# Kernel optimization log

Hardware: AMD Instinct MI355X
Metric: run time of the kernel (lower is better)

Reference implementation:

```python
import jax, jax.numpy as jnp
import numpy as np

B, N1, N2, C1, C2, MLP_OUT = 16, 4096, 1024, 128, 256, 256


def setup_inputs() -> dict:
    key = jax.random.key(0)
    k = jax.random.split(key, 8)
    xyz1 = jax.random.normal(k[0], (B, N1, 3), dtype=jnp.float32)
    feat1 = jax.random.normal(k[1], (B, N1, C1), dtype=jnp.float32)
    xyz2 = jax.random.normal(k[2], (B, N2, 3), dtype=jnp.float32)
    feat2 = jax.random.normal(k[3], (B, N2, C2), dtype=jnp.float32)
    d_in = C1 + C2
    W1 = jax.random.normal(k[4], (d_in, MLP_OUT), dtype=jnp.float32) / np.sqrt(d_in)
    b1 = jnp.zeros((MLP_OUT,), dtype=jnp.float32)
    W2 = jax.random.normal(k[5], (MLP_OUT, MLP_OUT), dtype=jnp.float32) / np.sqrt(MLP_OUT)
    b2 = jnp.zeros((MLP_OUT,), dtype=jnp.float32)
    return {"xyz1": xyz1, "feat1": feat1, "xyz2": xyz2, "feat2": feat2,
            "W1": W1, "b1": b1, "W2": W2, "b2": b2}


def reference(xyz1, feat1, xyz2, feat2, W1, b1, W2, b2):
    # squared pairwise distances [B, N1, N2]
    dists = jnp.sum((xyz1[:, :, None, :] - xyz2[:, None, :, :]) ** 2, axis=-1)
    # 3 nearest neighbors (smallest distances)
    neg_d3, idx = jax.lax.top_k(-dists, 3)      # [B, N1, 3]
    d3 = jnp.maximum(-neg_d3, 1e-10)
    w = 1.0 / d3
    w = w / jnp.sum(w, axis=-1, keepdims=True)   # [B, N1, 3]
    # gather neighbor features: [B, N1, 3, C2]
    neighbor_feats = jax.vmap(lambda f, i: f[i])(feat2, idx)
    interpolated = jnp.sum(w[..., None] * neighbor_feats, axis=2)  # [B, N1, C2]
    new_feat = jnp.concatenate([interpolated, feat1], axis=-1)     # [B, N1, C2+C1]
    h = jax.nn.relu(new_feat @ W1 + b1)
    return jax.nn.relu(h @ W2 + b2)
```

## Files before the change

kernel.cpp:

```cpp
#include <hip/hip_runtime.h>
#include <cstdint>
#include <cstddef>

typedef unsigned short ushort_t;
typedef unsigned int uint_t;

typedef __bf16 bf16x8 __attribute__((ext_vector_type(8)));
typedef float floatx4 __attribute__((ext_vector_type(4)));

#define B_ 16
#define N1_ 4096
#define N2_ 1024
#define C1_ 128
#define C2_ 256
#define DIN_ 384
#define DOUT_ 256
#define M_ (B_ * N1_)


__device__ __forceinline__ ushort_t f2bf(float f) {
  unsigned int u = __builtin_bit_cast(unsigned int, f);
  u = (u + 0x7fffu + ((u >> 16) & 1u)) >> 16;
  return (ushort_t)u;
}


__global__ __launch_bounds__(256) void prep_kernel(
    const float* __restrict__ W1, const float* __restrict__ W2,
    ushort_t* __restrict__ W1s, ushort_t* __restrict__ W2s) {
  int e = blockIdx.x * 256 + threadIdx.x;
  if (e < DOUT_ * DIN_) {
    int kk = e & 31, n = (e >> 5) & 255, t = e >> 13;
    W1s[e] = f2bf(W1[(size_t)(t * 32 + kk) * DOUT_ + n]);
  }
  if (e < DOUT_ * DOUT_) {
    int kk = e & 31, n = (e >> 5) & 255, t = e >> 13;
    W2s[e] = f2bf(W2[(size_t)(t * 32 + kk) * DOUT_ + n]);
  }
}


__device__ __forceinline__ void ins_exact(float& s0, float& s1, float& s2,
                                          int& i0, int& i1, int& i2,
                                          float d, int p) {
  float ns2 = __builtin_amdgcn_fmed3f(d, s1, s2);
  float ns1 = __builtin_amdgcn_fmed3f(d, s0, s1);
  float ns0 = fminf(d, s0);
  bool c0 = d < s0, c1 = d < s1, c2 = d < s2;
  i2 = c1 ? i1 : (c2 ? p : i2);
  i1 = c0 ? i0 : (c1 ? p : i1);
  i0 = c0 ? p : i0;
  s0 = ns0; s1 = ns1; s2 = ns2;
}

__device__ __forceinline__ void ins_merge(float& s0, float& s1, float& s2,
                                          int& i0, int& i1, int& i2,
                                          float e, int j) {
  bool t0 = (e < s0) || (e == s0 && j < i0);
  bool t1 = (e < s1) || (e == s1 && j < i1);
  bool t2 = (e < s2) || (e == s2 && j < i2);
  s2 = t1 ? s1 : (t2 ? e : s2);
  i2 = t1 ? i1 : (t2 ? j : i2);
  s1 = t0 ? s0 : (t1 ? e : s1);
  i1 = t0 ? i0 : (t1 ? j : i1);
  s0 = t0 ? e : s0;
  i0 = t0 ? j : i0;
}

__global__ __launch_bounds__(256) void knn_kernel(
    const float* __restrict__ xyz1, const float* __restrict__ xyz2,
    int* __restrict__ idx_out, float* __restrict__ w_out) {
  __shared__ float4 xs4[N2_];
  int b = blockIdx.x >> 6;
  int n1base = (blockIdx.x & 63) << 6;
  const float* p2 = xyz2 + (size_t)b * N2_ * 3;
  for (int i = threadIdx.x; i < N2_; i += 256) {
    const float* s = p2 + 3 * i;
    xs4[i] = make_float4(s[0], s[1], s[2], 0.0f);
  }
  __syncthreads();

  int g = threadIdx.x >> 3;
  int sub = threadIdx.x & 7;
  int rowA = b * N1_ + n1base + g;
  int rowB = rowA + 32;
  const float* pa = xyz1 + (size_t)rowA * 3;
  const float* pb = xyz1 + (size_t)rowB * 3;
  float ax = pa[0], ay = pa[1], az = pa[2];
  float bx = pb[0], by = pb[1], bz = pb[2];

  float as0 = 3.0e38f, as1 = 3.0e38f, as2 = 3.0e38f;
  float bs0 = 3.0e38f, bs1 = 3.0e38f, bs2 = 3.0e38f;
  int ai0 = 0, ai1 = 0, ai2 = 0;
  int bi0 = 0, bi1 = 0, bi2 = 0;

  int p = sub;
#pragma unroll 8
  for (int t = 0; t < N2_ / 8; ++t) {
    float4 qv = xs4[p];
    {
      float dx = ax - qv.x, dy = ay - qv.y, dz = az - qv.z;
      float d = dx * dx + dy * dy + dz * dz;
      ins_exact(as0, as1, as2, ai0, ai1, ai2, d, p);
    }
    {
      float dx = bx - qv.x, dy = by - qv.y, dz = bz - qv.z;
      float d = dx * dx + dy * dy + dz * dz;
      ins_exact(bs0, bs1, bs2, bi0, bi1, bi2, d, p);
    }
    p += 8;
  }

#pragma unroll
  for (int mm = 1; mm <= 4; mm <<= 1) {
    {
      float e0 = __shfl_xor(as0, mm), e1 = __shfl_xor(as1, mm), e2 = __shfl_xor(as2, mm);
      int j0 = __shfl_xor(ai0, mm), j1 = __shfl_xor(ai1, mm), j2 = __shfl_xor(ai2, mm);
      ins_merge(as0, as1, as2, ai0, ai1, ai2, e0, j0);
      ins_merge(as0, as1, as2, ai0, ai1, ai2, e1, j1);
      ins_merge(as0, as1, as2, ai0, ai1, ai2, e2, j2);
    }
    {
      float e0 = __shfl_xor(bs0, mm), e1 = __shfl_xor(bs1, mm), e2 = __shfl_xor(bs2, mm);
      int j0 = __shfl_xor(bi0, mm), j1 = __shfl_xor(bi1, mm), j2 = __shfl_xor(bi2, mm);
      ins_merge(bs0, bs1, bs2, bi0, bi1, bi2, e0, j0);
      ins_merge(bs0, bs1, bs2, bi0, bi1, bi2, e1, j1);
      ins_merge(bs0, bs1, bs2, bi0, bi1, bi2, e2, j2);
    }
  }

  if (sub == 0) {
    {
      float r0 = 1.0f / fmaxf(as0, 1e-10f);
      float r1 = 1.0f / fmaxf(as1, 1e-10f);
      float r2 = 1.0f / fmaxf(as2, 1e-10f);
      float s = 1.0f / (r0 + r1 + r2);
      int base = rowA * 3;
      idx_out[base + 0] = ai0;
      idx_out[base + 1] = ai1;
      idx_out[base + 2] = ai2;
      w_out[base + 0] = r0 * s;
      w_out[base + 1] = r1 * s;
      w_out[base + 2] = r2 * s;
    }
    {
      float r0 = 1.0f / fmaxf(bs0, 1e-10f);
      float r1 = 1.0f / fmaxf(bs1, 1e-10f);
      float r2 = 1.0f / fmaxf(bs2, 1e-10f);
      float s = 1.0f / (r0 + r1 + r2);
      int base = rowB * 3;
      idx_out[base + 0] = bi0;
      idx_out[base + 1] = bi1;
      idx_out[base + 2] = bi2;
      w_out[base + 0] = r0 * s;
      w_out[base + 1] = r1 * s;
      w_out[base + 2] = r2 * s;
    }
  }
}


__global__ __launch_bounds__(256, 2) void fused_kernel(
    const float* __restrict__ feat1, const float* __restrict__ feat2,
    const int* __restrict__ idx, const float* __restrict__ w,
    const ushort_t* __restrict__ W1s, const float* __restrict__ b1,
    const ushort_t* __restrict__ W2s, const float* __restrict__ b2,
    float* __restrict__ out) {
  __shared__ ushort_t As[64 * 384];
  const int tid = threadIdx.x;
  const int wave = tid >> 6;
  const int lane = tid & 63;
  const int m = lane & 15;
  const int q = lane >> 4;
  const int row0 = blockIdx.x * 64;
  const int b = row0 >> 12;

#pragma unroll 4
  for (int it = 0; it < 16; ++it) {
    int rl = wave * 16 + it;
    int row = row0 + rl;
    const int* ip = idx + (size_t)row * 3;
    const float* wp = w + (size_t)row * 3;
    int i0 = ip[0], i1 = ip[1], i2 = ip[2];
    float w0 = wp[0], w1 = wp[1], w2 = wp[2];

    const float4* f0 = (const float4*)(feat2 + ((size_t)b * N2_ + i0) * C2_);
    const float4* f1 = (const float4*)(feat2 + ((size_t)b * N2_ + i1) * C2_);
    const float4* f2 = (const float4*)(feat2 + ((size_t)b * N2_ + i2) * C2_);
    float4 a = f0[lane];
    float4 c = f1[lane];
    float4 d = f2[lane];
    float vx = w0 * a.x + w1 * c.x + w2 * d.x;
    float vy = w0 * a.y + w1 * c.y + w2 * d.y;
    float vz = w0 * a.z + w1 * c.z + w2 * d.z;
    float vw = w0 * a.w + w1 * c.w + w2 * d.w;
    uint_t lo = (uint_t)f2bf(vx) | ((uint_t)f2bf(vy) << 16);
    uint_t hi = (uint_t)f2bf(vz) | ((uint_t)f2bf(vw) << 16);
    int e = (lane >> 3) * 2048 + rl * 32 + ((4 * lane) & 31);
    *(uint2*)&As[e] = make_uint2(lo, hi);

    float2 t1 = ((const float2*)(feat1 + (size_t)row * C1_))[lane];
    uint_t pk = (uint_t)f2bf(t1.x) | ((uint_t)f2bf(t1.y) << 16);
    int e1 = (8 + (lane >> 4)) * 2048 + rl * 32 + ((2 * lane) & 31);
    *(uint_t*)&As[e1] = pk;
  }
  __syncthreads();

  const int b_off = (wave * 64 + m) * 32 + q * 8;
  const int a_base = m * 32 + q * 8;

  floatx4 acc[4][4];
#pragma unroll
  for (int i = 0; i < 4; ++i)
#pragma unroll
    for (int j = 0; j < 4; ++j) acc[i][j] = (floatx4)0.0f;

  {
    bf16x8 bf0[4], bf1[4], af[4];
#pragma unroll
    for (int j = 0; j < 4; ++j)
      bf0[j] = *(const bf16x8*)(W1s + b_off + j * 512);
#pragma unroll
    for (int t = 0; t < 12; t += 2) {
#pragma unroll
      for (int j = 0; j < 4; ++j)
        bf1[j] = *(const bf16x8*)(W1s + (size_t)(t + 1) * 8192 + b_off + j * 512);
#pragma unroll
      for (int i = 0; i < 4; ++i)
        af[i] = *(const bf16x8*)&As[t * 2048 + a_base + i * 512];
#pragma unroll
      for (int i = 0; i < 4; ++i)
#pragma unroll
        for (int j = 0; j < 4; ++j)
          acc[i][j] = __builtin_amdgcn_mfma_f32_16x16x32_bf16(af[i], bf0[j],
                                                              acc[i][j], 0, 0, 0);
      if (t + 2 < 12) {
#pragma unroll
        for (int j = 0; j < 4; ++j)
          bf0[j] = *(const bf16x8*)(W1s + (size_t)(t + 2) * 8192 + b_off + j * 512);
      }
#pragma unroll
      for (int i = 0; i < 4; ++i)
        af[i] = *(const bf16x8*)&As[(t + 1) * 2048 + a_base + i * 512];
#pragma unroll
      for (int i = 0; i < 4; ++i)
#pragma unroll
        for (int j = 0; j < 4; ++j)
          acc[i][j] = __builtin_amdgcn_mfma_f32_16x16x32_bf16(af[i], bf1[j],
                                                              acc[i][j], 0, 0, 0);
    }
  }
  __syncthreads();

  ushort_t* HS = As;
#pragma unroll
  for (int j = 0; j < 4; ++j) {
    int col = wave * 64 + j * 16 + m;
    float bv = b1[col];
    int cb = (col >> 3) & 3;
    int tb = (col >> 5) * 2048 + (col & 7);
#pragma unroll
    for (int i = 0; i < 4; ++i)
#pragma unroll
      for (int r = 0; r < 4; ++r) {
        int row = i * 16 + q * 4 + r;
        float v = acc[i][j][r] + bv;
        v = v > 0.0f ? v : 0.0f;
        int ch = cb ^ ((row >> 2) & 3);
        HS[tb + row * 32 + ch * 8] = f2bf(v);
      }
  }
  __syncthreads();

  floatx4 acc2[4][4];
#pragma unroll
  for (int i = 0; i < 4; ++i)
#pragma unroll
    for (int j = 0; j < 4; ++j) acc2[i][j] = (floatx4)0.0f;

  {
    bf16x8 bf0[4], bf1[4], af[4];
#pragma unroll
    for (int j = 0; j < 4; ++j)
      bf0[j] = *(const bf16x8*)(W2s + b_off + j * 512);
#pragma unroll
    for (int t = 0; t < 8; t += 2) {
#pragma unroll
      for (int j = 0; j < 4; ++j)
        bf1[j] = *(const bf16x8*)(W2s + (size_t)(t + 1) * 8192 + b_off + j * 512);
#pragma unroll
      for (int i = 0; i < 4; ++i) {
        int row = m + 16 * i;
        int ch = q ^ ((row >> 2) & 3);
        af[i] = *(const bf16x8*)&HS[t * 2048 + row * 32 + ch * 8];
      }
#pragma unroll
      for (int i = 0; i < 4; ++i)
#pragma unroll
        for (int j = 0; j < 4; ++j)
          acc2[i][j] = __builtin_amdgcn_mfma_f32_16x16x32_bf16(af[i], bf0[j],
                                                               acc2[i][j], 0, 0, 0);
      if (t + 2 < 8) {
#pragma unroll
        for (int j = 0; j < 4; ++j)
          bf0[j] = *(const bf16x8*)(W2s + (size_t)(t + 2) * 8192 + b_off + j * 512);
      }
#pragma unroll
      for (int i = 0; i < 4; ++i) {
        int row = m + 16 * i;
        int ch = q ^ ((row >> 2) & 3);
        af[i] = *(const bf16x8*)&HS[(t + 1) * 2048 + row * 32 + ch * 8];
      }
#pragma unroll
      for (int i = 0; i < 4; ++i)
#pragma unroll
        for (int j = 0; j < 4; ++j)
          acc2[i][j] = __builtin_amdgcn_mfma_f32_16x16x32_bf16(af[i], bf1[j],
                                                               acc2[i][j], 0, 0, 0);
    }
  }

#pragma unroll
  for (int j = 0; j < 4; ++j) {
    int col = wave * 64 + j * 16 + m;
    float bv = b2[col];
#pragma unroll
    for (int i = 0; i < 4; ++i)
#pragma unroll
      for (int r = 0; r < 4; ++r) {
        int row = i * 16 + q * 4 + r;
        float v = acc2[i][j][r] + bv;
        v = v > 0.0f ? v : 0.0f;
        out[(size_t)(row0 + row) * DOUT_ + col] = v;
      }
  }
}


constexpr size_t OFF_W1S = 0;
constexpr size_t OFF_W2S = OFF_W1S + 196608;
constexpr size_t OFF_IDX = OFF_W2S + 131072;
constexpr size_t OFF_W = OFF_IDX + 786432;
constexpr size_t WS_TOTAL = OFF_W + 786432;

extern "C" void kernel_launch(void* const* d_in, const int* in_sizes, int n_in,
                              void* d_out, int out_size, void* d_ws, size_t ws_size,
                              hipStream_t stream) {
  const float* xyz1 = (const float*)d_in[0];
  const float* feat1 = (const float*)d_in[1];
  const float* xyz2 = (const float*)d_in[2];
  const float* feat2 = (const float*)d_in[3];
  const float* W1 = (const float*)d_in[4];
  const float* b1 = (const float*)d_in[5];
  const float* W2 = (const float*)d_in[6];
  const float* b2 = (const float*)d_in[7];

  if (ws_size < WS_TOTAL) return;

  char* ws = (char*)d_ws;
  ushort_t* W1s = (ushort_t*)(ws + OFF_W1S);
  ushort_t* W2s = (ushort_t*)(ws + OFF_W2S);
  int* idx = (int*)(ws + OFF_IDX);
  float* w = (float*)(ws + OFF_W);

  prep_kernel<<<384, 256, 0, stream>>>(W1, W2, W1s, W2s);
  knn_kernel<<<B_ * (N1_ / 64), 256, 0, stream>>>(xyz1, xyz2, idx, w);
  fused_kernel<<<M_ / 64, 256, 0, stream>>>(feat1, feat2, idx, w, W1s, b1, W2s,
                                            b2, (float*)d_out);
}
```

Baseline: 194.7 us.

## Fuse KNN search into the MLP kernel, keeping neighbor indices in LDS

The separate KNN kernel is removed and its search runs at the start of the fused gather+MLP kernel. The xyz2 points are staged in the shared A-tile buffer, and the resulting indices and weights are kept in LDS instead of a global workspace. This removes one launch and the global round trip for idx and weights. Each block now runs the distance scan before its GEMM work, which lengthens the kernel and may change occupancy because LDS use grows slightly. The xyz2 load is also vectorized to float4 and the scan's unroll drops from 8 to 4.

```diff
diff --git a/kernel.cpp b/kernel.cpp
--- a/kernel.cpp
+++ b/kernel.cpp
@@ -67,106 +67,17 @@
   i0 = t0 ? j : i0;
 }
 
-__global__ __launch_bounds__(256) void knn_kernel(
+
+__global__ __launch_bounds__(256, 2) void fused_kernel(
     const float* __restrict__ xyz1, const float* __restrict__ xyz2,
-    int* __restrict__ idx_out, float* __restrict__ w_out) {
-  __shared__ float4 xs4[N2_];
-  int b = blockIdx.x >> 6;
-  int n1base = (blockIdx.x & 63) << 6;
-  const float* p2 = xyz2 + (size_t)b * N2_ * 3;
-  for (int i = threadIdx.x; i < N2_; i += 256) {
-    const float* s = p2 + 3 * i;
-    xs4[i] = make_float4(s[0], s[1], s[2], 0.0f);
-  }
-  __syncthreads();
-
-  int g = threadIdx.x >> 3;
-  int sub = threadIdx.x & 7;
-  int rowA = b * N1_ + n1base + g;
-  int rowB = rowA + 32;
-  const float* pa = xyz1 + (size_t)rowA * 3;
-  const float* pb = xyz1 + (size_t)rowB * 3;
-  float ax = pa[0], ay = pa[1], az = pa[2];
-  float bx = pb[0], by = pb[1], bz = pb[2];
-
-  float as0 = 3.0e38f, as1 = 3.0e38f, as2 = 3.0e38f;
-  float bs0 = 3.0e38f, bs1 = 3.0e38f, bs2 = 3.0e38f;
-  int ai0 = 0, ai1 = 0, ai2 = 0;
-  int bi0 = 0, bi1 = 0, bi2 = 0;
-
-  int p = sub;
-#pragma unroll 8
-  for (int t = 0; t < N2_ / 8; ++t) {
-    float4 qv = xs4[p];
-    {
-      float dx = ax - qv.x, dy = ay - qv.y, dz = az - qv.z;
-      float d = dx * dx + dy * dy + dz * dz;
-      ins_exact(as0, as1, as2, ai0, ai1, ai2, d, p);
-    }
-    {
-      float dx = bx - qv.x, dy = by - qv.y, dz = bz - qv.z;
-      float d = dx * dx + dy * dy + dz * dz;
-      ins_exact(bs0, bs1, bs2, bi0, bi1, bi2, d, p);
-    }
-    p += 8;
-  }
-
-#pragma unroll
-  for (int mm = 1; mm <= 4; mm <<= 1) {
-    {
-      float e0 = __shfl_xor(as0, mm), e1 = __shfl_xor(as1, mm), e2 = __shfl_xor(as2, mm);
-      int j0 = __shfl_xor(ai0, mm), j1 = __shfl_xor(ai1, mm), j2 = __shfl_xor(ai2, mm);
-      ins_merge(as0, as1, as2, ai0, ai1, ai2, e0, j0);
-      ins_merge(as0, as1, as2, ai0, ai1, ai2, e1, j1);
-      ins_merge(as0, as1, as2, ai0, ai1, ai2, e2, j2);
-    }
-    {
-      float e0 = __shfl_xor(bs0, mm), e1 = __shfl_xor(bs1, mm), e2 = __shfl_xor(bs2, mm);
-      int j0 = __shfl_xor(bi0, mm), j1 = __shfl_xor(bi1, mm), j2 = __shfl_xor(bi2, mm);
-      ins_merge(bs0, bs1, bs2, bi0, bi1, bi2, e0, j0);
-      ins_merge(bs0, bs1, bs2, bi0, bi1, bi2, e1, j1);
-      ins_merge(bs0, bs1, bs2, bi0, bi1, bi2, e2, j2);
-    }
-  }
-
-  if (sub == 0) {
-    {
-      float r0 = 1.0f / fmaxf(as0, 1e-10f);
-      float r1 = 1.0f / fmaxf(as1, 1e-10f);
-      float r2 = 1.0f / fmaxf(as2, 1e-10f);
-      float s = 1.0f / (r0 + r1 + r2);
-      int base = rowA * 3;
-      idx_out[base + 0] = ai0;
-      idx_out[base + 1] = ai1;
-      idx_out[base + 2] = ai2;
-      w_out[base + 0] = r0 * s;
-      w_out[base + 1] = r1 * s;
-      w_out[base + 2] = r2 * s;
-    }
-    {
-      float r0 = 1.0f / fmaxf(bs0, 1e-10f);
-      float r1 = 1.0f / fmaxf(bs1, 1e-10f);
-      float r2 = 1.0f / fmaxf(bs2, 1e-10f);
-      float s = 1.0f / (r0 + r1 + r2);
-      int base = rowB * 3;
-      idx_out[base + 0] = bi0;
-      idx_out[base + 1] = bi1;
-      idx_out[base + 2] = bi2;
-      w_out[base + 0] = r0 * s;
-      w_out[base + 1] = r1 * s;
-      w_out[base + 2] = r2 * s;
-    }
-  }
-}
-
-
-__global__ __launch_bounds__(256, 2) void fused_kernel(
     const float* __restrict__ feat1, const float* __restrict__ feat2,
-    const int* __restrict__ idx, const float* __restrict__ w,
     const ushort_t* __restrict__ W1s, const float* __restrict__ b1,
     const ushort_t* __restrict__ W2s, const float* __restrict__ b2,
     float* __restrict__ out) {
-  __shared__ ushort_t As[64 * 384];
+  __shared__ __align__(16) ushort_t As[64 * 384];
+  __shared__ int idxL[64 * 3];
+  __shared__ float wL[64 * 3];
+
   const int tid = threadIdx.x;
   const int wave = tid >> 6;
   const int lane = tid & 63;
@@ -175,14 +86,85 @@
   const int row0 = blockIdx.x * 64;
   const int b = row0 >> 12;
 
+  float4* xs4 = (float4*)As;
+  {
+    const float4* p24 = (const float4*)(xyz2 + (size_t)b * (N2_ * 3));
+    float4 A = p24[3 * tid + 0];
+    float4 Bv = p24[3 * tid + 1];
+    float4 Cv = p24[3 * tid + 2];
+    xs4[4 * tid + 0] = make_float4(A.x, A.y, A.z, 0.0f);
+    xs4[4 * tid + 1] = make_float4(A.w, Bv.x, Bv.y, 0.0f);
+    xs4[4 * tid + 2] = make_float4(Bv.z, Bv.w, Cv.x, 0.0f);
+    xs4[4 * tid + 3] = make_float4(Cv.y, Cv.z, Cv.w, 0.0f);
+  }
+  __syncthreads();
+
+  {
+    const int g = tid >> 3;
+    const int sub = tid & 7;
+    const float* pa = xyz1 + (size_t)(row0 + g) * 3;
+    const float* pb = xyz1 + (size_t)(row0 + g + 32) * 3;
+    float ax = pa[0], ay = pa[1], az = pa[2];
+    float bx = pb[0], by = pb[1], bz = pb[2];
+    float as0 = 3.0e38f, as1 = 3.0e38f, as2 = 3.0e38f;
+    float bs0 = 3.0e38f, bs1 = 3.0e38f, bs2 = 3.0e38f;
+    int ai0 = 0, ai1 = 0, ai2 = 0, bi0 = 0, bi1 = 0, bi2 = 0;
+    int p = sub;
+#pragma unroll 4
+    for (int t = 0; t < N2_ / 8; ++t) {
+      float4 qv = xs4[p];
+      {
+        float dx = ax - qv.x, dy = ay - qv.y, dz = az - qv.z;
+        float d = dx * dx + dy * dy + dz * dz;
+        ins_exact(as0, as1, as2, ai0, ai1, ai2, d, p);
+      }
+      {
+        float dx = bx - qv.x, dy = by - qv.y, dz = bz - qv.z;
+        float d = dx * dx + dy * dy + dz * dz;
+        ins_exact(bs0, bs1, bs2, bi0, bi1, bi2, d, p);
+      }
+      p += 8;
+    }
+#pragma unroll
+    for (int mm = 1; mm <= 4; mm <<= 1) {
+      {
+        float e0 = __shfl_xor(as0, mm), e1 = __shfl_xor(as1, mm), e2 = __shfl_xor(as2, mm);
+        int j0 = __shfl_xor(ai0, mm), j1 = __shfl_xor(ai1, mm), j2 = __shfl_xor(ai2, mm);
+        ins_merge(as0, as1, as2, ai0, ai1, ai2, e0, j0);
+        ins_merge(as0, as1, as2, ai0, ai1, ai2, e1, j1);
+        ins_merge(as0, as1, as2, ai0, ai1, ai2, e2, j2);
+      }
+      {
+        float e0 = __shfl_xor(bs0, mm), e1 = __shfl_xor(bs1, mm), e2 = __shfl_xor(bs2, mm);
+        int j0 = __shfl_xor(bi0, mm), j1 = __shfl_xor(bi1, mm), j2 = __shfl_xor(bi2, mm);
+        ins_merge(bs0, bs1, bs2, bi0, bi1, bi2, e0, j0);
+        ins_merge(bs0, bs1, bs2, bi0, bi1, bi2, e1, j1);
+        ins_merge(bs0, bs1, bs2, bi0, bi1, bi2, e2, j2);
+      }
+    }
+    if (sub == 0) {
+      float r0 = 1.0f / fmaxf(as0, 1e-10f);
+      float r1 = 1.0f / fmaxf(as1, 1e-10f);
+      float r2 = 1.0f / fmaxf(as2, 1e-10f);
+      float s = 1.0f / (r0 + r1 + r2);
+      idxL[g * 3 + 0] = ai0; idxL[g * 3 + 1] = ai1; idxL[g * 3 + 2] = ai2;
+      wL[g * 3 + 0] = r0 * s; wL[g * 3 + 1] = r1 * s; wL[g * 3 + 2] = r2 * s;
+      r0 = 1.0f / fmaxf(bs0, 1e-10f);
+      r1 = 1.0f / fmaxf(bs1, 1e-10f);
+      r2 = 1.0f / fmaxf(bs2, 1e-10f);
+      s = 1.0f / (r0 + r1 + r2);
+      idxL[(g + 32) * 3 + 0] = bi0; idxL[(g + 32) * 3 + 1] = bi1; idxL[(g + 32) * 3 + 2] = bi2;
+      wL[(g + 32) * 3 + 0] = r0 * s; wL[(g + 32) * 3 + 1] = r1 * s; wL[(g + 32) * 3 + 2] = r2 * s;
+    }
+  }
+  __syncthreads();
+
 #pragma unroll 4
   for (int it = 0; it < 16; ++it) {
     int rl = wave * 16 + it;
     int row = row0 + rl;
-    const int* ip = idx + (size_t)row * 3;
-    const float* wp = w + (size_t)row * 3;
-    int i0 = ip[0], i1 = ip[1], i2 = ip[2];
-    float w0 = wp[0], w1 = wp[1], w2 = wp[2];
+    int i0 = idxL[rl * 3 + 0], i1 = idxL[rl * 3 + 1], i2 = idxL[rl * 3 + 2];
+    float w0 = wL[rl * 3 + 0], w1 = wL[rl * 3 + 1], w2 = wL[rl * 3 + 2];
 
     const float4* f0 = (const float4*)(feat2 + ((size_t)b * N2_ + i0) * C2_);
     const float4* f1 = (const float4*)(feat2 + ((size_t)b * N2_ + i1) * C2_);
@@ -339,9 +321,7 @@
 
 constexpr size_t OFF_W1S = 0;
 constexpr size_t OFF_W2S = OFF_W1S + 196608;
-constexpr size_t OFF_IDX = OFF_W2S + 131072;
-constexpr size_t OFF_W = OFF_IDX + 786432;
-constexpr size_t WS_TOTAL = OFF_W + 786432;
+constexpr size_t WS_TOTAL = OFF_W2S + 131072;
 
 extern "C" void kernel_launch(void* const* d_in, const int* in_sizes, int n_in,
                               void* d_out, int out_size, void* d_ws, size_t ws_size,
@@ -360,11 +340,8 @@
   char* ws = (char*)d_ws;
   ushort_t* W1s = (ushort_t*)(ws + OFF_W1S);
   ushort_t* W2s = (ushort_t*)(ws + OFF_W2S);
-  int* idx = (int*)(ws + OFF_IDX);
-  float* w = (float*)(ws + OFF_W);
 
   prep_kernel<<<384, 256, 0, stream>>>(W1, W2, W1s, W2s);
-  knn_kernel<<<B_ * (N1_ / 64), 256, 0, stream>>>(xyz1, xyz2, idx, w);
-  fused_kernel<<<M_ / 64, 256, 0, stream>>>(feat1, feat2, idx, w, W1s, b1, W2s,
-                                            b2, (float*)d_out);
-}
+  fused_kernel<<<M_ / 64, 256, 0, stream>>>(xyz1, xyz2, feat1, feat2, W1s, b1,
+                                            W2s, b2, (float*)d_out);
+}
```

After: 192.9 us. About the same (-0.9%).
